# Kernel tuning notes

Hardware: AMD Instinct MI355X
Metric: run time of the kernel (lower is better)

Reference implementation:

```python
import jax, jax.numpy as jnp
import numpy as np

N = 100000   # nodes (batched graph)
E = 1600000  # edges
G = 2048     # molecules in the batch
D_IN = 128
D_H = 128
MLP_H = 512


def setup_inputs() -> dict:
    key = jax.random.key(0)
    ks = jax.random.split(key, 20)

    def w(k, i, o):
        return (jax.random.normal(k, (i, o), jnp.float32) / np.sqrt(i)).astype(jnp.float32)

    feats = jax.random.normal(ks[0], (N, D_IN), jnp.float32)
    src = jax.random.randint(ks[1], (E,), 0, N)
    dst = jax.random.randint(ks[2], (E,), 0, N)
    graph_ids = jnp.sort(jax.random.randint(ks[3], (N,), 0, G))

    return {
        "feats": feats, "src": src, "dst": dst, "graph_ids": graph_ids,
        # 3 GraphConv layers
        "W0": w(ks[4], D_IN, D_H), "b0": jnp.zeros((D_H,), jnp.float32),
        "W1": w(ks[5], D_H, D_H),  "b1": jnp.zeros((D_H,), jnp.float32),
        "W2": w(ks[6], D_H, D_H),  "b2": jnp.zeros((D_H,), jnp.float32),
        # MLP head: D_H -> 512 -> 256 -> 1
        "Wm0": w(ks[7], D_H, MLP_H),       "bm0": jnp.zeros((MLP_H,), jnp.float32),
        "Wm1": w(ks[8], MLP_H, MLP_H // 2), "bm1": jnp.zeros((MLP_H // 2,), jnp.float32),
        "Wm2": w(ks[9], MLP_H // 2, 1),     "bm2": jnp.zeros((1,), jnp.float32),
    }


def reference(feats, src, dst, graph_ids, W0, b0, W1, b1, W2, b2,
              Wm0, bm0, Wm1, bm1, Wm2, bm2):
    ones_e = jnp.ones((E,), jnp.float32)
    # DGL GraphConv norm='both': D_out^{-1/2} on src, D_in^{-1/2} on dst; deg clamped to 1
    deg_out = jnp.maximum(jax.ops.segment_sum(ones_e, src, num_segments=N), 1.0)
    deg_in = jnp.maximum(jax.ops.segment_sum(ones_e, dst, num_segments=N), 1.0)
    inv_src = jax.lax.rsqrt(deg_out)[:, None]
    inv_dst = jax.lax.rsqrt(deg_in)[:, None]

    def gcn_layer(h, W, b):
        h = h * inv_src                                   # [N, D]
        m = jax.ops.segment_sum(h[src], dst, num_segments=N)  # gather-scatter over edges
        m = m * inv_dst
        return jax.nn.relu(jnp.dot(m, W) + b)

    h = gcn_layer(feats, W0, b0)
    h = gcn_layer(h, W1, b1)
    h = gcn_layer(h, W2, b2)

    # AvgPooling per graph
    counts = jnp.maximum(jax.ops.segment_sum(jnp.ones((N,), jnp.float32), graph_ids, num_segments=G), 1.0)
    emb = jax.ops.segment_sum(h, graph_ids, num_segments=G) / counts[:, None]  # [G, D_H]

    # MLP head (dropout = identity in eval)
    x = jax.nn.relu(jnp.dot(emb, Wm0) + bm0)
    x = jax.nn.relu(jnp.dot(x, Wm1) + bm1)
    return jnp.dot(x, Wm2) + bm2  # [G, 1]
```

## Files before the change

kernel.cpp:

```cpp
#include <hip/hip_runtime.h>


static inline int ceil_div(int a, int b){ return (a + b - 1) / b; }

#define B1 128
#define NBMAX 1024

typedef __bf16 bf16x8 __attribute__((ext_vector_type(8)));
typedef float  f32x4  __attribute__((ext_vector_type(4)));

__global__ __launch_bounds__(256) void bucket_count_kernel(
    const int* __restrict__ src, const int* __restrict__ dst,
    unsigned* __restrict__ cntA, unsigned* __restrict__ cntB,
    int E, int NB){
  __shared__ unsigned la[NBMAX], lb[NBMAX];
  int t = threadIdx.x;
  for (int i = t; i < NB; i += 256){ la[i] = 0u; lb[i] = 0u; }
  __syncthreads();
  int chunk = (E + B1 - 1) / B1;
  int e0 = blockIdx.x * chunk, e1 = min(e0 + chunk, E);
  for (int e = e0 + t; e < e1; e += 256){
    atomicAdd(&la[dst[e] >> 7], 1u);
    atomicAdd(&lb[src[e] >> 7], 1u);
  }
  __syncthreads();
  for (int i = t; i < NB; i += 256){
    cntA[(size_t)blockIdx.x * NB + i] = la[i];
    cntB[(size_t)blockIdx.x * NB + i] = lb[i];
  }
}

__global__ void scan_cols_kernel(unsigned* __restrict__ cntA, unsigned* __restrict__ cntB,
                                 unsigned* __restrict__ totals, int NB){
  int b = blockIdx.x * 256 + threadIdx.x;
  if (b >= NB) return;
  unsigned* cnt = blockIdx.y ? cntB : cntA;
  unsigned run = 0;
  for (int blk = 0; blk < B1; blk++){
    unsigned v = cnt[(size_t)blk * NB + b];
    cnt[(size_t)blk * NB + b] = run;
    run += v;
  }
  totals[(size_t)blockIdx.y * NB + b] = run;
}

__global__ void scan_base_kernel(const unsigned* __restrict__ totals,
                                 unsigned* __restrict__ baseA, unsigned* __restrict__ baseB,
                                 int NB, int E){
  __shared__ unsigned s[NBMAX];
  int t = threadIdx.x;
  for (int job = 0; job < 2; job++){
    unsigned* base = job ? baseB : baseA;
    unsigned x = (t < NB) ? totals[(size_t)job * NB + t] : 0u;
    s[t] = x;
    __syncthreads();
    for (int off = 1; off < NBMAX; off <<= 1){
      unsigned v = (t >= off) ? s[t - off] : 0u;
      __syncthreads();
      s[t] += v;
      __syncthreads();
    }
    if (t < NB) base[t] = s[t] - x;
    if (t == 0) base[NB] = (unsigned)E;
    __syncthreads();
  }
}

__global__ __launch_bounds__(256) void bucket_scatter_kernel(
    const int* __restrict__ src, const int* __restrict__ dst,
    const unsigned* __restrict__ cntA, const unsigned* __restrict__ cntB,
    const unsigned* __restrict__ baseA, const unsigned* __restrict__ baseB,
    unsigned* __restrict__ bpack_d, unsigned char* __restrict__ bsrc_s,
    int E, int NB){
  __shared__ unsigned curA[NBMAX], curB[NBMAX];
  int t = threadIdx.x;
  for (int i = t; i < NB; i += 256){
    curA[i] = baseA[i] + cntA[(size_t)blockIdx.x * NB + i];
    curB[i] = baseB[i] + cntB[(size_t)blockIdx.x * NB + i];
  }
  __syncthreads();
  int chunk = (E + B1 - 1) / B1;
  int e0 = blockIdx.x * chunk, e1 = min(e0 + chunk, E);
  for (int e = e0 + t; e < e1; e += 256){
    int s = src[e], d = dst[e];
    unsigned p = atomicAdd(&curA[d >> 7], 1u);
    bpack_d[p] = ((unsigned)(d & 127) << 17) | (unsigned)s;
    unsigned q = atomicAdd(&curB[s >> 7], 1u);
    bsrc_s[q] = (unsigned char)(s & 127);
  }
}

__global__ __launch_bounds__(256) void csr_finalize_kernel(
    const unsigned* __restrict__ bpack_d, const unsigned* __restrict__ baseA,
    int* __restrict__ row_ptr, float* __restrict__ inv_dst, int* __restrict__ col,
    int N, int E, int NB){
  __shared__ unsigned cnt[128];
  __shared__ unsigned scn[128];
  int b = blockIdx.x, t = threadIdx.x;
  int node0 = b << 7;
  int nn = min(128, N - node0);
  int e0 = (int)baseA[b], e1 = (int)baseA[b + 1];
  if (t < 128) cnt[t] = 0u;
  __syncthreads();
  for (int e = e0 + t; e < e1; e += 256)
    atomicAdd(&cnt[(bpack_d[e] >> 17) & 127u], 1u);
  __syncthreads();
  unsigned mycnt = (t < 128) ? cnt[t] : 0u;
  if (t < 128) scn[t] = mycnt;
  __syncthreads();
  for (int off = 1; off < 128; off <<= 1){
    unsigned v = (t < 128 && t >= off) ? scn[t - off] : 0u;
    __syncthreads();
    if (t < 128) scn[t] += v;
    __syncthreads();
  }
  if (t < nn){
    unsigned excl = scn[t] - mycnt;
    row_ptr[node0 + t] = e0 + (int)excl;
    unsigned c = mycnt < 1u ? 1u : mycnt;
    inv_dst[node0 + t] = rsqrtf((float)c);
    cnt[t] = (unsigned)e0 + excl;
  }
  if (b == NB - 1 && t == 0) row_ptr[N] = E;
  __syncthreads();
  for (int e = e0 + t; e < e1; e += 256){
    unsigned v = bpack_d[e];
    unsigned p = atomicAdd(&cnt[(v >> 17) & 127u], 1u);
    col[p] = (int)(v & 0x1FFFFu);
  }
}

__global__ __launch_bounds__(256) void degout_finalize_kernel(
    const unsigned char* __restrict__ bsrc_s, const unsigned* __restrict__ baseB,
    float* __restrict__ inv_src, int N){
  __shared__ unsigned cnt[128];
  int b = blockIdx.x, t = threadIdx.x;
  int node0 = b << 7;
  int nn = min(128, N - node0);
  int e0 = (int)baseB[b], e1 = (int)baseB[b + 1];
  if (t < 128) cnt[t] = 0u;
  __syncthreads();
  for (int e = e0 + t; e < e1; e += 256)
    atomicAdd(&cnt[bsrc_s[e]], 1u);
  __syncthreads();
  if (t < nn){
    unsigned c = cnt[t] < 1u ? 1u : cnt[t];
    inv_src[node0 + t] = rsqrtf((float)c);
  }
}

__global__ void scale_rows_kernel(const float* __restrict__ in, const float* __restrict__ sc,
                                  float* __restrict__ out, int n4){
  int i = blockIdx.x*blockDim.x + threadIdx.x;
  if (i < n4){
    float4 v = ((const float4*)in)[i];
    float s = sc[i >> 5];
    v.x *= s; v.y *= s; v.z *= s; v.w *= s;
    ((float4*)out)[i] = v;
  }
}

__global__ __launch_bounds__(256) void csr_agg_kernel(
    const int* __restrict__ row_ptr, const int* __restrict__ col,
    const float* __restrict__ hs, float* __restrict__ agg, int N){
  int node = (int)((blockIdx.x*256u + threadIdx.x) >> 5);
  int lane = threadIdx.x & 31;
  if (node >= N) return;
  int r0 = row_ptr[node];
  int r1 = row_ptr[node+1];
  float4 a0 = make_float4(0.f,0.f,0.f,0.f);
  float4 a1 = make_float4(0.f,0.f,0.f,0.f);
  float4 a2 = make_float4(0.f,0.f,0.f,0.f);
  float4 a3 = make_float4(0.f,0.f,0.f,0.f);
  int e = r0;
  for (; e + 3 < r1; e += 4){
    int s0 = col[e], s1 = col[e+1], s2 = col[e+2], s3 = col[e+3];
    float4 v0 = ((const float4*)(hs + (size_t)s0*128))[lane];
    float4 v1 = ((const float4*)(hs + (size_t)s1*128))[lane];
    float4 v2 = ((const float4*)(hs + (size_t)s2*128))[lane];
    float4 v3 = ((const float4*)(hs + (size_t)s3*128))[lane];
    a0.x += v0.x; a0.y += v0.y; a0.z += v0.z; a0.w += v0.w;
    a1.x += v1.x; a1.y += v1.y; a1.z += v1.z; a1.w += v1.w;
    a2.x += v2.x; a2.y += v2.y; a2.z += v2.z; a2.w += v2.w;
    a3.x += v3.x; a3.y += v3.y; a3.z += v3.z; a3.w += v3.w;
  }
  for (; e < r1; e++){
    int s0 = col[e];
    float4 v0 = ((const float4*)(hs + (size_t)s0*128))[lane];
    a0.x += v0.x; a0.y += v0.y; a0.z += v0.z; a0.w += v0.w;
  }
  float4 r;
  r.x = (a0.x + a1.x) + (a2.x + a3.x);
  r.y = (a0.y + a1.y) + (a2.y + a3.y);
  r.z = (a0.z + a1.z) + (a2.z + a3.z);
  r.w = (a0.w + a1.w) + (a2.w + a3.w);
  ((float4*)(agg + (size_t)node*128))[lane] = r;
}

__global__ void wprep_kernel(const float* __restrict__ W,
                             __bf16* __restrict__ Whi, __bf16* __restrict__ Wlo){
  int idx = blockIdx.x*256 + threadIdx.x;
  if (idx >= 128*128) return;
  int k = idx >> 7, n = idx & 127;
  float w = W[idx];
  __bf16 h = (__bf16)w;
  __bf16 l = (__bf16)(w - (float)h);
  Whi[n*128 + k] = h;
  Wlo[n*128 + k] = l;
}

__global__ __launch_bounds__(256) void mfma_gemm_kernel(
    const float* __restrict__ A,
    const __bf16* __restrict__ Whi, const __bf16* __restrict__ Wlo,
    const float* __restrict__ bias, const float* __restrict__ row_scale,
    const float* __restrict__ out_scale, float* __restrict__ out, int M){
  const int tid  = threadIdx.x;
  const int wv   = tid >> 6;
  const int lane = tid & 63;
  const int q    = lane >> 4;
  const int mn   = lane & 15;
  const int row0 = blockIdx.x*128 + wv*32;

  f32x4 acc[2][8];
  #pragma unroll
  for (int mt = 0; mt < 2; mt++)
    #pragma unroll
    for (int nt = 0; nt < 8; nt++)
      acc[mt][nt] = (f32x4){0.f,0.f,0.f,0.f};

  float rs[2];
  #pragma unroll
  for (int mt = 0; mt < 2; mt++){
    int ridx = row0 + mt*16 + mn;
    if (ridx >= M) ridx = M - 1;
    rs[mt] = row_scale ? row_scale[ridx] : 1.f;
  }

  #pragma unroll
  for (int kc = 0; kc < 4; kc++){
    bf16x8 ah[2], al[2];
    #pragma unroll
    for (int mt = 0; mt < 2; mt++){
      const float* ap = A + (size_t)(row0 + mt*16 + mn)*128 + kc*32 + q*8;
      float4 x0 = *(const float4*)ap;
      float4 x1 = *(const float4*)(ap + 4);
      float v[8] = {x0.x, x0.y, x0.z, x0.w, x1.x, x1.y, x1.z, x1.w};
      #pragma unroll
      for (int j = 0; j < 8; j++){
        float s = v[j] * rs[mt];
        __bf16 h = (__bf16)s;
        ah[mt][j] = h;
        al[mt][j] = (__bf16)(s - (float)h);
      }
    }
    #pragma unroll
    for (int nt = 0; nt < 8; nt++){
      size_t boff = (size_t)(nt*16 + mn)*128 + kc*32 + q*8;
      bf16x8 bh = *(const bf16x8*)(Whi + boff);
      bf16x8 bl = *(const bf16x8*)(Wlo + boff);
      #pragma unroll
      for (int mt = 0; mt < 2; mt++){
        acc[mt][nt] = __builtin_amdgcn_mfma_f32_16x16x32_bf16(al[mt], bh, acc[mt][nt], 0, 0, 0);
        acc[mt][nt] = __builtin_amdgcn_mfma_f32_16x16x32_bf16(ah[mt], bl, acc[mt][nt], 0, 0, 0);
        acc[mt][nt] = __builtin_amdgcn_mfma_f32_16x16x32_bf16(ah[mt], bh, acc[mt][nt], 0, 0, 0);
      }
    }
  }

  #pragma unroll
  for (int mt = 0; mt < 2; mt++){
    #pragma unroll
    for (int r = 0; r < 4; r++){
      int gm = row0 + mt*16 + q*4 + r;
      if (gm < M){
        float osc = out_scale ? out_scale[gm] : 1.f;
        #pragma unroll
        for (int nt = 0; nt < 8; nt++){
          float v = acc[mt][nt][r] + bias[nt*16 + mn];
          v = fmaxf(v, 0.f) * osc;
          out[(size_t)gm*128 + nt*16 + mn] = v;
        }
      }
    }
  }
}

__global__ __launch_bounds__(256) void gemm_kernel(
    const float* __restrict__ A, const float* __restrict__ W,
    const float* __restrict__ bias, const float* __restrict__ row_scale,
    const float* __restrict__ out_scale, float* __restrict__ out,
    int M, int K, int Ncols, int do_relu){
  __shared__ float As[32][68];
  __shared__ float Bs[32][128];

  const int tid = threadIdx.x;
  const int tx = tid & 31;
  const int ty = tid >> 5;
  const int row0 = blockIdx.x * 64;
  const int col0 = blockIdx.y * 128;

  float acc[8][4];
  #pragma unroll
  for (int i = 0; i < 8; i++)
    #pragma unroll
    for (int j = 0; j < 4; j++) acc[i][j] = 0.f;

  for (int kb = 0; kb < K; kb += 32){
    #pragma unroll
    for (int i = 0; i < 2; i++){
      int flat = i*256 + tid;
      int m = flat >> 3, k4 = (flat & 7) << 2;
      int gm = row0 + m;
      float4 v = make_float4(0.f, 0.f, 0.f, 0.f);
      if (gm < M){
        v = *(const float4*)(A + (size_t)gm*K + kb + k4);
        if (row_scale){ float s = row_scale[gm]; v.x*=s; v.y*=s; v.z*=s; v.w*=s; }
      }
      As[k4+0][m] = v.x; As[k4+1][m] = v.y; As[k4+2][m] = v.z; As[k4+3][m] = v.w;
    }
    #pragma unroll
    for (int i = 0; i < 4; i++){
      int flat = i*256 + tid;
      int k = flat >> 5, j4 = (flat & 31) << 2;
      float4 v = *(const float4*)(W + (size_t)(kb + k)*Ncols + col0 + j4);
      *(float4*)&Bs[k][j4] = v;
    }
    __syncthreads();
    #pragma unroll
    for (int k = 0; k < 32; k++){
      float4 b = *(const float4*)&Bs[k][tx << 2];
      float a[8];
      #pragma unroll
      for (int i = 0; i < 8; i++) a[i] = As[k][ty*8 + i];
      #pragma unroll
      for (int i = 0; i < 8; i++){
        acc[i][0] = fmaf(a[i], b.x, acc[i][0]);
        acc[i][1] = fmaf(a[i], b.y, acc[i][1]);
        acc[i][2] = fmaf(a[i], b.z, acc[i][2]);
        acc[i][3] = fmaf(a[i], b.w, acc[i][3]);
      }
    }
    __syncthreads();
  }

  float4 bi = *(const float4*)(bias + col0 + (tx << 2));
  #pragma unroll
  for (int i = 0; i < 8; i++){
    int gm = row0 + ty*8 + i;
    if (gm < M){
      float4 v;
      v.x = acc[i][0] + bi.x; v.y = acc[i][1] + bi.y;
      v.z = acc[i][2] + bi.z; v.w = acc[i][3] + bi.w;
      if (do_relu){
        v.x = fmaxf(v.x, 0.f); v.y = fmaxf(v.y, 0.f);
        v.z = fmaxf(v.z, 0.f); v.w = fmaxf(v.w, 0.f);
      }
      if (out_scale){ float s = out_scale[gm]; v.x*=s; v.y*=s; v.z*=s; v.w*=s; }
      *(float4*)(out + (size_t)gm*Ncols + col0 + (tx << 2)) = v;
    }
  }
}

__global__ void pool_kernel(const float* __restrict__ h, const int* __restrict__ gid,
                            float* __restrict__ emb, int N, int G){
  int g = blockIdx.x;
  int lane = threadIdx.x;
  int lo = 0, hi = N;
  while (lo < hi){ int mid = (lo + hi) >> 1; if (gid[mid] < g) lo = mid + 1; else hi = mid; }
  int start = lo;
  hi = N;
  while (lo < hi){ int mid = (lo + hi) >> 1; if (gid[mid] <= g) lo = mid + 1; else hi = mid; }
  int end = lo;
  float ax = 0.f, ay = 0.f;
  for (int n = start; n < end; n++){
    float2 v = ((const float2*)(h + (size_t)n*128))[lane];
    ax += v.x; ay += v.y;
  }
  int c = end - start; if (c < 1) c = 1;
  float invc = 1.0f / (float)c;
  float2 r; r.x = ax * invc; r.y = ay * invc;
  ((float2*)(emb + (size_t)g*128))[lane] = r;
}

__global__ void final_dot_kernel(const float* __restrict__ x, const float* __restrict__ w,
                                 const float* __restrict__ b, float* __restrict__ out, int G){
  int idx = blockIdx.x*blockDim.x + threadIdx.x;
  int g = idx >> 6, lane = idx & 63;
  if (g >= G) return;
  float4 xv = ((const float4*)(x + (size_t)g*256))[lane];
  float4 wv = ((const float4*)w)[lane];
  float s = xv.x*wv.x + xv.y*wv.y + xv.z*wv.z + xv.w*wv.w;
  for (int off = 32; off > 0; off >>= 1) s += __shfl_down(s, off);
  if (lane == 0) out[g] = s + b[0];
}

extern "C" void kernel_launch(void* const* d_in, const int* in_sizes, int n_in,
                              void* d_out, int out_size, void* d_ws, size_t ws_size,
                              hipStream_t stream){
  const float* feats = (const float*)d_in[0];
  const int*   src   = (const int*)d_in[1];
  const int*   dst   = (const int*)d_in[2];
  const int*   gid   = (const int*)d_in[3];
  const float* W0 = (const float*)d_in[4];   const float* b0 = (const float*)d_in[5];
  const float* W1 = (const float*)d_in[6];   const float* b1 = (const float*)d_in[7];
  const float* W2 = (const float*)d_in[8];   const float* b2 = (const float*)d_in[9];
  const float* Wm0 = (const float*)d_in[10]; const float* bm0 = (const float*)d_in[11];
  const float* Wm1 = (const float*)d_in[12]; const float* bm1 = (const float*)d_in[13];
  const float* Wm2 = (const float*)d_in[14]; const float* bm2 = (const float*)d_in[15];
  float* out = (float*)d_out;

  const int E   = in_sizes[1];
  const int N   = in_sizes[3];
  const int G   = out_size;
  const int MH  = in_sizes[11];
  const int MH2 = in_sizes[13];
  const int NB  = ceil_div(N, 128);

  char* ws = (char*)d_ws;
  size_t off = 0;
  auto carve = [&](size_t bytes) -> char* {
    off = (off + 255) & ~(size_t)255;
    char* p = ws + off; off += bytes; return p;
  };
  float* inv_src = (float*)carve((size_t)N*4);
  float* inv_dst = (float*)carve((size_t)N*4);
  int* row_ptr = (int*)carve((size_t)(N+1)*4);
  int* col     = (int*)carve((size_t)E*4);
  __bf16* Wsp[6];
  for (int i = 0; i < 6; i++) Wsp[i] = (__bf16*)carve(128*128*2);
  float* hs  = (float*)carve((size_t)N*128*4);
  float* agg = (float*)carve((size_t)N*128*4);
  float* emb = (float*)carve((size_t)G*128*4);
  float* x1  = (float*)carve((size_t)G*MH*4);
  float* x2  = (float*)carve((size_t)G*MH2*4);

  unsigned* T = (unsigned*)agg;
  unsigned* cntA   = T;
  unsigned* cntB   = cntA + (size_t)B1*NB;
  unsigned* totals = cntB + (size_t)B1*NB;
  unsigned* baseA  = totals + 2*(size_t)NB;
  unsigned* baseB  = baseA + (NB+1);
  unsigned* bpack_d = baseB + (NB+1);
  unsigned char* bsrc_s = (unsigned char*)(bpack_d + E);

  bucket_count_kernel<<<B1, 256, 0, stream>>>(src, dst, cntA, cntB, E, NB);
  scan_cols_kernel<<<dim3(ceil_div(NB,256), 2), 256, 0, stream>>>(cntA, cntB, totals, NB);
  scan_base_kernel<<<1, NBMAX, 0, stream>>>(totals, baseA, baseB, NB, E);
  bucket_scatter_kernel<<<B1, 256, 0, stream>>>(src, dst, cntA, cntB, baseA, baseB,
                                                bpack_d, bsrc_s, E, NB);
  csr_finalize_kernel<<<NB, 256, 0, stream>>>(bpack_d, baseA, row_ptr, inv_dst, col, N, E, NB);
  degout_finalize_kernel<<<NB, 256, 0, stream>>>(bsrc_s, baseB, inv_src, N);
  wprep_kernel<<<64, 256, 0, stream>>>(W0, Wsp[0], Wsp[1]);
  wprep_kernel<<<64, 256, 0, stream>>>(W1, Wsp[2], Wsp[3]);
  wprep_kernel<<<64, 256, 0, stream>>>(W2, Wsp[4], Wsp[5]);
  scale_rows_kernel<<<ceil_div(N*32,256), 256, 0, stream>>>(feats, inv_src, hs, N*32);

  const int agg_blocks = ceil_div(N*32, 256);
  const int ggrid = ceil_div(N, 128);
  csr_agg_kernel<<<agg_blocks, 256, 0, stream>>>(row_ptr, col, hs, agg, N);
  mfma_gemm_kernel<<<ggrid, 256, 0, stream>>>(agg, Wsp[0], Wsp[1], b0, inv_dst, inv_src, hs, N);
  csr_agg_kernel<<<agg_blocks, 256, 0, stream>>>(row_ptr, col, hs, agg, N);
  mfma_gemm_kernel<<<ggrid, 256, 0, stream>>>(agg, Wsp[2], Wsp[3], b1, inv_dst, inv_src, hs, N);
  csr_agg_kernel<<<agg_blocks, 256, 0, stream>>>(row_ptr, col, hs, agg, N);
  mfma_gemm_kernel<<<ggrid, 256, 0, stream>>>(agg, Wsp[4], Wsp[5], b2, inv_dst, nullptr, hs, N);
  pool_kernel<<<G, 64, 0, stream>>>(hs, gid, emb, N, G);
  gemm_kernel<<<dim3(ceil_div(G,64), MH/128),  256, 0, stream>>>(emb, Wm0, bm0, nullptr, nullptr, x1, G, 128, MH, 1);
  gemm_kernel<<<dim3(ceil_div(G,64), MH2/128), 256, 0, stream>>>(x1, Wm1, bm1, nullptr, nullptr, x2, G, MH, MH2, 1);
  final_dot_kernel<<<ceil_div(G*64,256), 256, 0, stream>>>(x2, Wm2, bm2, out, G);
}
```

Baseline: 804.6 us.

## Fuse scaling and bf16 split into aggregation, merge setup kernels

Removes the separate scale_rows pass: the first aggregation reads the raw features and applies inv_src per gathered neighbour. The aggregation kernel now applies inv_dst and pre-splits each output into packed hi/lo bf16 words, so the GEMM only unpacks bits instead of scaling and converting. The degree-out finalize is merged into csr_finalize, the three weight-prep launches become one, and the bucket block count B1 goes from 128 to 256. This cuts launches and one full N×128 read/write pass, at the cost of an extra scale load per gathered edge in layer 0.

```diff
diff --git a/kernel.cpp b/kernel.cpp
--- a/kernel.cpp
+++ b/kernel.cpp
@@ -3,11 +3,23 @@
 
 static inline int ceil_div(int a, int b){ return (a + b - 1) / b; }
 
-#define B1 128
+#define B1 256
 #define NBMAX 1024
 
 typedef __bf16 bf16x8 __attribute__((ext_vector_type(8)));
 typedef float  f32x4  __attribute__((ext_vector_type(4)));
+
+static __device__ inline __bf16 bits_to_bf16(unsigned short u){
+  union { unsigned short u; __bf16 b; } x; x.u = u; return x.b;
+}
+static __device__ inline unsigned short bf16_bits(__bf16 b){
+  union { __bf16 b; unsigned short u; } x; x.b = b; return x.u;
+}
+static __device__ inline unsigned pack_split(float s){
+  __bf16 h = (__bf16)s;
+  __bf16 l = (__bf16)(s - (float)h);
+  return ((unsigned)bf16_bits(h) << 16) | (unsigned)bf16_bits(l);
+}
 
 __global__ __launch_bounds__(256) void bucket_count_kernel(
     const int* __restrict__ src, const int* __restrict__ dst,
@@ -91,9 +103,10 @@
 }
 
 __global__ __launch_bounds__(256) void csr_finalize_kernel(
-    const unsigned* __restrict__ bpack_d, const unsigned* __restrict__ baseA,
-    int* __restrict__ row_ptr, float* __restrict__ inv_dst, int* __restrict__ col,
-    int N, int E, int NB){
+    const unsigned* __restrict__ bpack_d, const unsigned char* __restrict__ bsrc_s,
+    const unsigned* __restrict__ baseA, const unsigned* __restrict__ baseB,
+    int* __restrict__ row_ptr, float* __restrict__ inv_dst, float* __restrict__ inv_src,
+    int* __restrict__ col, int N, int E, int NB){
   __shared__ unsigned cnt[128];
   __shared__ unsigned scn[128];
   int b = blockIdx.x, t = threadIdx.x;
@@ -128,19 +141,11 @@
     unsigned p = atomicAdd(&cnt[(v >> 17) & 127u], 1u);
     col[p] = (int)(v & 0x1FFFFu);
   }
-}
-
-__global__ __launch_bounds__(256) void degout_finalize_kernel(
-    const unsigned char* __restrict__ bsrc_s, const unsigned* __restrict__ baseB,
-    float* __restrict__ inv_src, int N){
-  __shared__ unsigned cnt[128];
-  int b = blockIdx.x, t = threadIdx.x;
-  int node0 = b << 7;
-  int nn = min(128, N - node0);
-  int e0 = (int)baseB[b], e1 = (int)baseB[b + 1];
+  __syncthreads();
   if (t < 128) cnt[t] = 0u;
   __syncthreads();
-  for (int e = e0 + t; e < e1; e += 256)
+  int f0 = (int)baseB[b], f1 = (int)baseB[b + 1];
+  for (int e = f0 + t; e < f1; e += 256)
     atomicAdd(&cnt[bsrc_s[e]], 1u);
   __syncthreads();
   if (t < nn){
@@ -149,20 +154,11 @@
   }
 }
 
-__global__ void scale_rows_kernel(const float* __restrict__ in, const float* __restrict__ sc,
-                                  float* __restrict__ out, int n4){
-  int i = blockIdx.x*blockDim.x + threadIdx.x;
-  if (i < n4){
-    float4 v = ((const float4*)in)[i];
-    float s = sc[i >> 5];
-    v.x *= s; v.y *= s; v.z *= s; v.w *= s;
-    ((float4*)out)[i] = v;
-  }
-}
-
+template<bool SC>
 __global__ __launch_bounds__(256) void csr_agg_kernel(
     const int* __restrict__ row_ptr, const int* __restrict__ col,
-    const float* __restrict__ hs, float* __restrict__ agg, int N){
+    const float* __restrict__ hs, const float* __restrict__ scale,
+    const float* __restrict__ inv_dst, unsigned* __restrict__ aggp, int N){
   int node = (int)((blockIdx.x*256u + threadIdx.x) >> 5);
   int lane = threadIdx.x & 31;
   if (node >= N) return;
@@ -179,6 +175,13 @@
     float4 v1 = ((const float4*)(hs + (size_t)s1*128))[lane];
     float4 v2 = ((const float4*)(hs + (size_t)s2*128))[lane];
     float4 v3 = ((const float4*)(hs + (size_t)s3*128))[lane];
+    if (SC){
+      float c0 = scale[s0], c1 = scale[s1], c2 = scale[s2], c3 = scale[s3];
+      v0.x*=c0; v0.y*=c0; v0.z*=c0; v0.w*=c0;
+      v1.x*=c1; v1.y*=c1; v1.z*=c1; v1.w*=c1;
+      v2.x*=c2; v2.y*=c2; v2.z*=c2; v2.w*=c2;
+      v3.x*=c3; v3.y*=c3; v3.z*=c3; v3.w*=c3;
+    }
     a0.x += v0.x; a0.y += v0.y; a0.z += v0.z; a0.w += v0.w;
     a1.x += v1.x; a1.y += v1.y; a1.z += v1.z; a1.w += v1.w;
     a2.x += v2.x; a2.y += v2.y; a2.z += v2.z; a2.w += v2.w;
@@ -187,33 +190,40 @@
   for (; e < r1; e++){
     int s0 = col[e];
     float4 v0 = ((const float4*)(hs + (size_t)s0*128))[lane];
+    if (SC){ float c0 = scale[s0]; v0.x*=c0; v0.y*=c0; v0.z*=c0; v0.w*=c0; }
     a0.x += v0.x; a0.y += v0.y; a0.z += v0.z; a0.w += v0.w;
   }
-  float4 r;
-  r.x = (a0.x + a1.x) + (a2.x + a3.x);
-  r.y = (a0.y + a1.y) + (a2.y + a3.y);
-  r.z = (a0.z + a1.z) + (a2.z + a3.z);
-  r.w = (a0.w + a1.w) + (a2.w + a3.w);
-  ((float4*)(agg + (size_t)node*128))[lane] = r;
-}
-
-__global__ void wprep_kernel(const float* __restrict__ W,
-                             __bf16* __restrict__ Whi, __bf16* __restrict__ Wlo){
-  int idx = blockIdx.x*256 + threadIdx.x;
-  if (idx >= 128*128) return;
+  float idst = inv_dst[node];
+  float rx = ((a0.x + a1.x) + (a2.x + a3.x)) * idst;
+  float ry = ((a0.y + a1.y) + (a2.y + a3.y)) * idst;
+  float rz = ((a0.z + a1.z) + (a2.z + a3.z)) * idst;
+  float rw = ((a0.w + a1.w) + (a2.w + a3.w)) * idst;
+  uint4 p;
+  p.x = pack_split(rx); p.y = pack_split(ry);
+  p.z = pack_split(rz); p.w = pack_split(rw);
+  ((uint4*)(aggp + (size_t)node*128))[lane] = p;
+}
+
+__global__ void wprep_kernel(const float* __restrict__ W0, const float* __restrict__ W1,
+                             const float* __restrict__ W2,
+                             __bf16* __restrict__ Wsp){
+  int gidx = blockIdx.x*256 + threadIdx.x;
+  if (gidx >= 3*128*128) return;
+  int layer = gidx >> 14, idx = gidx & 16383;
+  const float* W = layer == 0 ? W0 : (layer == 1 ? W1 : W2);
   int k = idx >> 7, n = idx & 127;
   float w = W[idx];
   __bf16 h = (__bf16)w;
   __bf16 l = (__bf16)(w - (float)h);
-  Whi[n*128 + k] = h;
-  Wlo[n*128 + k] = l;
+  Wsp[(size_t)layer*2*16384 + n*128 + k] = h;
+  Wsp[(size_t)layer*2*16384 + 16384 + n*128 + k] = l;
 }
 
 __global__ __launch_bounds__(256) void mfma_gemm_kernel(
-    const float* __restrict__ A,
+    const unsigned* __restrict__ A,
     const __bf16* __restrict__ Whi, const __bf16* __restrict__ Wlo,
-    const float* __restrict__ bias, const float* __restrict__ row_scale,
-    const float* __restrict__ out_scale, float* __restrict__ out, int M){
+    const float* __restrict__ bias, const float* __restrict__ out_scale,
+    float* __restrict__ out, int M){
   const int tid  = threadIdx.x;
   const int wv   = tid >> 6;
   const int lane = tid & 63;
@@ -228,29 +238,19 @@
     for (int nt = 0; nt < 8; nt++)
       acc[mt][nt] = (f32x4){0.f,0.f,0.f,0.f};
 
-  float rs[2];
-  #pragma unroll
-  for (int mt = 0; mt < 2; mt++){
-    int ridx = row0 + mt*16 + mn;
-    if (ridx >= M) ridx = M - 1;
-    rs[mt] = row_scale ? row_scale[ridx] : 1.f;
-  }
-
   #pragma unroll
   for (int kc = 0; kc < 4; kc++){
     bf16x8 ah[2], al[2];
     #pragma unroll
     for (int mt = 0; mt < 2; mt++){
-      const float* ap = A + (size_t)(row0 + mt*16 + mn)*128 + kc*32 + q*8;
-      float4 x0 = *(const float4*)ap;
-      float4 x1 = *(const float4*)(ap + 4);
-      float v[8] = {x0.x, x0.y, x0.z, x0.w, x1.x, x1.y, x1.z, x1.w};
+      const unsigned* ap = A + (size_t)(row0 + mt*16 + mn)*128 + kc*32 + q*8;
+      uint4 x0 = *(const uint4*)ap;
+      uint4 x1 = *(const uint4*)(ap + 4);
+      unsigned v[8] = {x0.x, x0.y, x0.z, x0.w, x1.x, x1.y, x1.z, x1.w};
       #pragma unroll
       for (int j = 0; j < 8; j++){
-        float s = v[j] * rs[mt];
-        __bf16 h = (__bf16)s;
-        ah[mt][j] = h;
-        al[mt][j] = (__bf16)(s - (float)h);
+        ah[mt][j] = bits_to_bf16((unsigned short)(v[j] >> 16));
+        al[mt][j] = bits_to_bf16((unsigned short)(v[j] & 0xFFFFu));
       }
     }
     #pragma unroll
@@ -426,15 +426,14 @@
   float* inv_dst = (float*)carve((size_t)N*4);
   int* row_ptr = (int*)carve((size_t)(N+1)*4);
   int* col     = (int*)carve((size_t)E*4);
-  __bf16* Wsp[6];
-  for (int i = 0; i < 6; i++) Wsp[i] = (__bf16*)carve(128*128*2);
+  __bf16* Wsp = (__bf16*)carve(6*128*128*2);
   float* hs  = (float*)carve((size_t)N*128*4);
-  float* agg = (float*)carve((size_t)N*128*4);
+  unsigned* aggp = (unsigned*)carve((size_t)N*128*4);
   float* emb = (float*)carve((size_t)G*128*4);
   float* x1  = (float*)carve((size_t)G*MH*4);
   float* x2  = (float*)carve((size_t)G*MH2*4);
 
-  unsigned* T = (unsigned*)agg;
+  unsigned* T = (unsigned*)aggp;
   unsigned* cntA   = T;
   unsigned* cntB   = cntA + (size_t)B1*NB;
   unsigned* totals = cntB + (size_t)B1*NB;
@@ -448,21 +447,21 @@
   scan_base_kernel<<<1, NBMAX, 0, stream>>>(totals, baseA, baseB, NB, E);
   bucket_scatter_kernel<<<B1, 256, 0, stream>>>(src, dst, cntA, cntB, baseA, baseB,
                                                 bpack_d, bsrc_s, E, NB);
-  csr_finalize_kernel<<<NB, 256, 0, stream>>>(bpack_d, baseA, row_ptr, inv_dst, col, N, E, NB);
-  degout_finalize_kernel<<<NB, 256, 0, stream>>>(bsrc_s, baseB, inv_src, N);
-  wprep_kernel<<<64, 256, 0, stream>>>(W0, Wsp[0], Wsp[1]);
-  wprep_kernel<<<64, 256, 0, stream>>>(W1, Wsp[2], Wsp[3]);
-  wprep_kernel<<<64, 256, 0, stream>>>(W2, Wsp[4], Wsp[5]);
-  scale_rows_kernel<<<ceil_div(N*32,256), 256, 0, stream>>>(feats, inv_src, hs, N*32);
+  csr_finalize_kernel<<<NB, 256, 0, stream>>>(bpack_d, bsrc_s, baseA, baseB,
+                                              row_ptr, inv_dst, inv_src, col, N, E, NB);
+  wprep_kernel<<<192, 256, 0, stream>>>(W0, W1, W2, Wsp);
 
   const int agg_blocks = ceil_div(N*32, 256);
   const int ggrid = ceil_div(N, 128);
-  csr_agg_kernel<<<agg_blocks, 256, 0, stream>>>(row_ptr, col, hs, agg, N);
-  mfma_gemm_kernel<<<ggrid, 256, 0, stream>>>(agg, Wsp[0], Wsp[1], b0, inv_dst, inv_src, hs, N);
-  csr_agg_kernel<<<agg_blocks, 256, 0, stream>>>(row_ptr, col, hs, agg, N);
-  mfma_gemm_kernel<<<ggrid, 256, 0, stream>>>(agg, Wsp[2], Wsp[3], b1, inv_dst, inv_src, hs, N);
-  csr_agg_kernel<<<agg_blocks, 256, 0, stream>>>(row_ptr, col, hs, agg, N);
-  mfma_gemm_kernel<<<ggrid, 256, 0, stream>>>(agg, Wsp[4], Wsp[5], b2, inv_dst, nullptr, hs, N);
+  __bf16 *Whi0 = Wsp,            *Wlo0 = Wsp + 16384;
+  __bf16 *Whi1 = Wsp + 2*16384,  *Wlo1 = Wsp + 3*16384;
+  __bf16 *Whi2 = Wsp + 4*16384,  *Wlo2 = Wsp + 5*16384;
+  csr_agg_kernel<true><<<agg_blocks, 256, 0, stream>>>(row_ptr, col, feats, inv_src, inv_dst, aggp, N);
+  mfma_gemm_kernel<<<ggrid, 256, 0, stream>>>(aggp, Whi0, Wlo0, b0, inv_src, hs, N);
+  csr_agg_kernel<false><<<agg_blocks, 256, 0, stream>>>(row_ptr, col, hs, nullptr, inv_dst, aggp, N);
+  mfma_gemm_kernel<<<ggrid, 256, 0, stream>>>(aggp, Whi1, Wlo1, b1, inv_src, hs, N);
+  csr_agg_kernel<false><<<agg_blocks, 256, 0, stream>>>(row_ptr, col, hs, nullptr, inv_dst, aggp, N);
+  mfma_gemm_kernel<<<ggrid, 256, 0, stream>>>(aggp, Whi2, Wlo2, b2, nullptr, hs, N);
   pool_kernel<<<G, 64, 0, stream>>>(hs, gid, emb, N, G);
   gemm_kernel<<<dim3(ceil_div(G,64), MH/128),  256, 0, stream>>>(emb, Wm0, bm0, nullptr, nullptr, x1, G, 128, MH, 1);
   gemm_kernel<<<dim3(ceil_div(G,64), MH2/128), 256, 0, stream>>>(x1, Wm1, bm1, nullptr, nullptr, x2, G, MH, MH2, 1);
```

Result: no change. 789.7 us (-1.9%).
